# Performance work log

Hardware: AMD Instinct MI355X
Metric: run time of the kernel (lower is better)

## Reference

```python
import jax, jax.numpy as jnp
import numpy as np

N_HARMONICS = 100
SAMPLE_RATE = 44100
HOP_SIZE = 64
TWO_PI = 2.0 * np.pi


def setup_inputs() -> dict:
    key = jax.random.key(0)
    k1, k2, k3, k4 = jax.random.split(key, 4)
    B, T, H = 16, 500, N_HARMONICS
    f0 = jax.random.uniform(k1, (B, T, 1), dtype=jnp.float32)
    loudness = jax.random.uniform(k2, (B, T, 1), dtype=jnp.float32)
    harm_amps = jax.random.uniform(k3, (B, T, H), dtype=jnp.float32)
    harm_stretch = jax.random.uniform(k4, (B, T, 1), dtype=jnp.float32)
    return {"f0": f0, "loudness": loudness, "harm_amps": harm_amps,
            "harm_stretch": harm_stretch}


def reference(f0, loudness, harm_amps, harm_stretch):
    # harmonic indices 1..H (buffer in the torch module)
    h = jnp.arange(1, N_HARMONICS + 1, dtype=f0.dtype)  # [H]
    # prepare_harmonics
    harm = h ** (1.0 + harm_stretch)        # [B, T, H]
    harm = harm * f0                        # instantaneous harmonic freqs (Hz)
    nyquist = SAMPLE_RATE // 2
    amps = jnp.where(harm > nyquist, 0.0, harm_amps)  # in-place mask in torch
    w = harm * (TWO_PI / SAMPLE_RATE)       # radians per sample
    w = jnp.repeat(w, HOP_SIZE, axis=1)     # [B, T*hop, H]
    # generate_phases
    phases = jnp.cumsum(w, axis=1) % TWO_PI  # [B, T*hop, H]
    # generate_signal
    l = jnp.repeat(loudness, HOP_SIZE, axis=1)   # [B, T*hop, 1]
    a = jnp.repeat(amps, HOP_SIZE, axis=1)       # [B, T*hop, H]
    signal = jnp.sum(l * a * jnp.sin(phases), axis=2) / N_HARMONICS
    return signal  # [B, T*hop]
```

## Files before the change

### kernel.cpp

```cpp
#include <hip/hip_runtime.h>
#include <math.h>


#define OB_B 16
#define OB_T 500
#define OB_H 100
#define OB_HOP 64

constexpr double SR_D = 44100.0;

__device__ __forceinline__ float readlane_f(float v, int l) {
    return __builtin_bit_cast(float, __builtin_amdgcn_readlane(__builtin_bit_cast(int, v), l));
}

__global__ void __launch_bounds__(256)
ob_scan_fused(const float* __restrict__ f0,
              const float* __restrict__ stretch,
              float2* __restrict__ wb)
{
    int wave = threadIdx.x >> 6;
    int lane = threadIdx.x & 63;
    int bh   = blockIdx.x * 4 + wave;
    int b = bh / OB_H, h = bh % OB_H;
    double L = log2((double)(h + 1));
    const float* f0b = f0      + b * OB_T;
    const float* stb = stretch + b * OB_T;

    double w[8];
    double csum = 0.0;
    int t0 = lane * 8;
    #pragma unroll
    for (int k = 0; k < 8; ++k) {
        int t = t0 + k;
        double wv = 0.0;
        if (t < OB_T)
            wv = exp2((1.0 + (double)stb[t]) * L) * (double)f0b[t] * (1.0 / SR_D);
        w[k] = wv;
        csum += wv;
    }
    double incl = csum;
    #pragma unroll
    for (int off = 1; off < 64; off <<= 1) {
        double up = __shfl_up(incl, (unsigned)off, 64);
        if (lane >= off) incl += up;
    }
    double S = incl - csum;
    #pragma unroll
    for (int k = 0; k < 8; ++k) {
        int t = t0 + k;
        if (t < OB_T) {
            double ph = 64.0 * S;
            ph -= trunc(ph);
            wb[(size_t)(b * OB_T + t) * OB_H + h] = make_float2((float)w[k], (float)ph);
            S += w[k];
        }
    }
}

__global__ void __launch_bounds__(256)
ob_synth(const float2* __restrict__ wb,
         const float* __restrict__ amps,
         const float* __restrict__ loud,
         float* __restrict__ out)
{
    int wave = threadIdx.x >> 6;
    int lane = threadIdx.x & 63;
    int bt   = blockIdx.x * 4 + wave;
    const float2* row  = wb   + (size_t)bt * OB_H;
    const float*  arow = amps + (size_t)bt * OB_H;
    float ld = loud[bt] * (1.0f / OB_H);

    float2 wb0 = row[lane];
    float  c0  = (wb0.x > 0.5f) ? 0.0f : ld * arow[lane];
    float2 wb1 = make_float2(0.0f, 0.0f);
    float  c1  = 0.0f;
    if (lane < OB_H - 64) {
        wb1 = row[64 + lane];
        c1  = (wb1.x > 0.5f) ? 0.0f : ld * arow[64 + lane];
    }

    float jf  = (float)(lane + 1);
    float acc = 0.0f;
    #pragma unroll
    for (int h = 0; h < 64; ++h) {
        float w = readlane_f(wb0.x, h);
        float b = readlane_f(wb0.y, h);
        float c = readlane_f(c0,   h);
        acc += c * __builtin_amdgcn_sinf(b + jf * w);
    }
    #pragma unroll
    for (int h = 0; h < OB_H - 64; ++h) {
        float w = readlane_f(wb1.x, h);
        float b = readlane_f(wb1.y, h);
        float c = readlane_f(c1,   h);
        acc += c * __builtin_amdgcn_sinf(b + jf * w);
    }
    out[(size_t)bt * OB_HOP + lane] = acc;
}

extern "C" void kernel_launch(void* const* d_in, const int* in_sizes, int n_in,
                              void* d_out, int out_size, void* d_ws, size_t ws_size,
                              hipStream_t stream)
{
    const float* f0      = (const float*)d_in[0];
    const float* loud    = (const float*)d_in[1];
    const float* amps    = (const float*)d_in[2];
    const float* stretch = (const float*)d_in[3];

    float2* wbuf = (float2*)d_ws;
    float*  out  = (float*)d_out;

    ob_scan_fused<<<(OB_B * OB_H) / 4, 256, 0, stream>>>(f0, stretch, wbuf);
    ob_synth<<<(OB_B * OB_T) / 4, 256, 0, stream>>>(wbuf, amps, loud, out);
}
```

Baseline: 87.10 us.

## Fold amplitude masking into scan kernel and read uniform float4 rows in synth

The scan kernel now computes the masked, loudness-scaled amplitude coefficient and writes it alongside frequency and phase as a padded float4 per (b,t,h). The synth kernel drops the per-lane loads and readlane broadcasts, and instead has every lane load the same float4 row entry (a wave-uniform address) in a single loop over all harmonics. This removes the cross-lane broadcast instructions and the amps/loud reads from synth. In exchange the workspace traffic doubles (float4 versus float2), and the scan kernel does strided, uncoalesced amps reads with h as the fastest-varying store index.

```diff
diff --git a/kernel.cpp b/kernel.cpp
--- a/kernel.cpp
+++ b/kernel.cpp
@@ -9,14 +9,12 @@
 
 constexpr double SR_D = 44100.0;
 
-__device__ __forceinline__ float readlane_f(float v, int l) {
-    return __builtin_bit_cast(float, __builtin_amdgcn_readlane(__builtin_bit_cast(int, v), l));
-}
-
 __global__ void __launch_bounds__(256)
 ob_scan_fused(const float* __restrict__ f0,
+              const float* __restrict__ loud,
+              const float* __restrict__ amps,
               const float* __restrict__ stretch,
-              float2* __restrict__ wb)
+              float4* __restrict__ wbc)
 {
     int wave = threadIdx.x >> 6;
     int lane = threadIdx.x & 63;
@@ -25,6 +23,7 @@
     double L = log2((double)(h + 1));
     const float* f0b = f0      + b * OB_T;
     const float* stb = stretch + b * OB_T;
+    const float* ldb = loud    + b * OB_T;
 
     double w[8];
     double csum = 0.0;
@@ -51,49 +50,31 @@
         if (t < OB_T) {
             double ph = 64.0 * S;
             ph -= trunc(ph);
-            wb[(size_t)(b * OB_T + t) * OB_H + h] = make_float2((float)w[k], (float)ph);
+            int bt = b * OB_T + t;
+            float wf = (float)w[k];
+            float c  = (wf > 0.5f) ? 0.0f
+                       : ldb[t] * amps[(size_t)bt * OB_H + h] * (1.0f / OB_H);
+            wbc[(size_t)bt * OB_H + h] = make_float4(wf, (float)ph, c, 0.0f);
             S += w[k];
         }
     }
 }
 
 __global__ void __launch_bounds__(256)
-ob_synth(const float2* __restrict__ wb,
-         const float* __restrict__ amps,
-         const float* __restrict__ loud,
+ob_synth(const float4* __restrict__ wbc,
          float* __restrict__ out)
 {
     int wave = threadIdx.x >> 6;
     int lane = threadIdx.x & 63;
-    int bt   = blockIdx.x * 4 + wave;
-    const float2* row  = wb   + (size_t)bt * OB_H;
-    const float*  arow = amps + (size_t)bt * OB_H;
-    float ld = loud[bt] * (1.0f / OB_H);
-
-    float2 wb0 = row[lane];
-    float  c0  = (wb0.x > 0.5f) ? 0.0f : ld * arow[lane];
-    float2 wb1 = make_float2(0.0f, 0.0f);
-    float  c1  = 0.0f;
-    if (lane < OB_H - 64) {
-        wb1 = row[64 + lane];
-        c1  = (wb1.x > 0.5f) ? 0.0f : ld * arow[64 + lane];
-    }
+    int bt   = __builtin_amdgcn_readfirstlane(blockIdx.x * 4 + wave);
+    const float4* __restrict__ row = wbc + (size_t)bt * OB_H;
 
     float jf  = (float)(lane + 1);
     float acc = 0.0f;
-    #pragma unroll
-    for (int h = 0; h < 64; ++h) {
-        float w = readlane_f(wb0.x, h);
-        float b = readlane_f(wb0.y, h);
-        float c = readlane_f(c0,   h);
-        acc += c * __builtin_amdgcn_sinf(b + jf * w);
-    }
-    #pragma unroll
-    for (int h = 0; h < OB_H - 64; ++h) {
-        float w = readlane_f(wb1.x, h);
-        float b = readlane_f(wb1.y, h);
-        float c = readlane_f(c1,   h);
-        acc += c * __builtin_amdgcn_sinf(b + jf * w);
+    #pragma unroll 10
+    for (int h = 0; h < OB_H; ++h) {
+        float4 q = row[h];
+        acc += q.z * __builtin_amdgcn_sinf(q.y + jf * q.x);
     }
     out[(size_t)bt * OB_HOP + lane] = acc;
 }
@@ -107,9 +88,9 @@
     const float* amps    = (const float*)d_in[2];
     const float* stretch = (const float*)d_in[3];
 
-    float2* wbuf = (float2*)d_ws;
-    float*  out  = (float*)d_out;
+    float4* wbc = (float4*)d_ws;
+    float*  out = (float*)d_out;
 
-    ob_scan_fused<<<(OB_B * OB_H) / 4, 256, 0, stream>>>(f0, stretch, wbuf);
-    ob_synth<<<(OB_B * OB_T) / 4, 256, 0, stream>>>(wbuf, amps, loud, out);
+    ob_scan_fused<<<(OB_B * OB_H) / 4, 256, 0, stream>>>(f0, loud, amps, stretch, wbc);
+    ob_synth<<<(OB_B * OB_T) / 4, 256, 0, stream>>>(wbc, out);
 }
```

Result: no change. 87.45 us (+0.4%).
